# Performance work log

Measured on AMD Instinct MI355X. Metric: run time of the kernel, lower is better.

## Reference

```python
import jax, jax.numpy as jnp
import numpy as np

B, N, C = 8, 1024, 768
H, D = 12, 64  # num_heads, head_dim
SCALE = D ** -0.5


def setup_inputs() -> dict:
    key = jax.random.key(0)
    ks = jax.random.split(key, 6)
    x = jax.random.normal(ks[0], (B, N, C), dtype=jnp.float32)
    # per-head Linear weights stacked: [H, D, C] (torch Linear stores [out, in])
    Wq = jax.random.normal(ks[1], (H, D, C), dtype=jnp.float32) * 0.02
    Wk = jax.random.normal(ks[2], (H, D, C), dtype=jnp.float32) * 0.02
    Wv = jax.random.normal(ks[3], (H, D, C), dtype=jnp.float32) * 0.02
    Wp = jax.random.normal(ks[4], (C, C), dtype=jnp.float32) * 0.02
    bp = jnp.zeros((C,), dtype=jnp.float32)
    return {"x": x, "Wq": Wq, "Wk": Wk, "Wv": Wv, "Wp": Wp, "bp": bp}


def reference(x, Wq, Wk, Wv, Wp, bp):
    # Per-head projections (batched across heads): [B, H, N, D]
    q = jnp.einsum('bnc,hdc->bhnd', x, Wq) * SCALE
    k = jnp.einsum('bnc,hdc->bhnd', x, Wk)
    v = jnp.einsum('bnc,hdc->bhnd', x, Wv)
    # Scaled dot-product attention per head
    attn = jax.nn.softmax(jnp.einsum('bhnd,bhmd->bhnm', q, k), axis=-1)
    out = jnp.einsum('bhnm,bhmd->bhnd', attn, v)
    # Concat heads along last dim == transpose to [B, N, H, D] then reshape
    out = out.transpose(0, 2, 1, 3).reshape(x.shape[0], x.shape[1], -1)
    # Output projection
    return out @ Wp.T + bp
```

## Files before the change

kernel.cpp:

```cpp
#include <hip/hip_runtime.h>

typedef unsigned short u16;
typedef __attribute__((ext_vector_type(8))) __bf16 bf16x8;
typedef __attribute__((ext_vector_type(4))) float f32x4;

__device__ __forceinline__ u16 f2bf(float f) {
    union { float f; unsigned u; } v; v.f = f;
    unsigned u = v.u;
    u += 0x7FFFu + ((u >> 16) & 1u);
    return (u16)(u >> 16);
}

typedef const __attribute__((address_space(1))) void GV;
typedef __attribute__((address_space(3))) void LV;
__device__ __forceinline__ void gl2lds16(const void* g, void* l) {
    __builtin_amdgcn_global_load_lds((GV*)g, (LV*)l, 16, 0, 0);
}

__global__ __launch_bounds__(256) void cast_all(
    const float* __restrict__ x,  const float* __restrict__ Wq,
    const float* __restrict__ Wk, const float* __restrict__ Wv,
    const float* __restrict__ Wp,
    u16* __restrict__ xb, u16* __restrict__ wb, u16* __restrict__ wpb)
{
    int bid = blockIdx.x;
    const float4* s; ushort4* d; int idx;
    if (bid < 6144) {
        s = (const float4*)x; d = (ushort4*)xb; idx = bid * 256 + threadIdx.x;
    } else {
        int t = bid - 6144;
        int w = t / 576;
        idx = (t - w * 576) * 256 + threadIdx.x;
        s = (const float4*)(w == 0 ? Wq : w == 1 ? Wk : w == 2 ? Wv : Wp);
        d = (ushort4*)(w == 3 ? wpb : wb + w * 589824);
    }
    float4 f = s[idx];
    ushort4 o;
    o.x = f2bf(f.x); o.y = f2bf(f.y); o.z = f2bf(f.z); o.w = f2bf(f.w);
    d[idx] = o;
}

__device__ __forceinline__ void stage_tile64(const u16* src, int k0, u16* lds, int tid) {
    #pragma unroll
    for (int h = 0; h < 4; h++) {
        int i = h * 256 + tid;
        int row = i >> 3, p = i & 7;
        int l = p ^ (row & 7);
        gl2lds16(src + (size_t)row * 768 + k0 + l * 8, lds + i * 8);
    }
}
__device__ __forceinline__ const bf16x8* frag64(const u16* lds, int row, int kc) {
    return reinterpret_cast<const bf16x8*>(lds + row * 64 + ((kc ^ (row & 7)) * 8));
}

__global__ __launch_bounds__(256, 2) void gemm_qkv(
    const u16* __restrict__ A, const u16* __restrict__ Bm,
    u16* __restrict__ qo, u16* __restrict__ ko, u16* __restrict__ vto)
{
    __shared__ u16 As[8192];
    __shared__ u16 Bs[8192];
    const int tid = threadIdx.x;
    const int wave = tid >> 6, lane = tid & 63;
    const int quad = lane >> 4, l16 = lane & 15;
    const int wr = (wave >> 1) * 64, wc = (wave & 1) * 64;
    const int rowBase = blockIdx.y * 128;
    const int colBase = blockIdx.x * 128;

    f32x4 acc[4][4] = {};
    const u16* aSrc = A + (size_t)rowBase * 768;
    const u16* bSrc = Bm + (size_t)colBase * 768;

    for (int k0 = 0; k0 < 768; k0 += 64) {
        __syncthreads();
        stage_tile64(aSrc, k0, As, tid);
        stage_tile64(bSrc, k0, Bs, tid);
        __syncthreads();
        #pragma unroll
        for (int ks = 0; ks < 2; ks++) {
            bf16x8 a[4], b[4];
            #pragma unroll
            for (int mi = 0; mi < 4; mi++)
                a[mi] = *frag64(As, wr + mi * 16 + l16, ks * 4 + quad);
            #pragma unroll
            for (int ni = 0; ni < 4; ni++)
                b[ni] = *frag64(Bs, wc + ni * 16 + l16, ks * 4 + quad);
            #pragma unroll
            for (int mi = 0; mi < 4; mi++)
                #pragma unroll
                for (int ni = 0; ni < 4; ni++)
                    acc[mi][ni] = __builtin_amdgcn_mfma_f32_16x16x32_bf16(a[mi], b[ni], acc[mi][ni], 0, 0, 0);
        }
    }

    #pragma unroll
    for (int mi = 0; mi < 4; mi++) {
        #pragma unroll
        for (int ni = 0; ni < 4; ni++) {
            int gj = colBase + wc + ni * 16 + l16;
            int which = gj / 768;
            int r = gj - which * 768;
            int h = r >> 6, d = r & 63;
            int gi0 = rowBase + wr + mi * 16 + quad * 4;
            int b_ = gi0 >> 10;
            int n0 = gi0 & 1023;
            if (which == 2) {
                ushort4 pk;
                pk.x = f2bf(acc[mi][ni][0]);
                pk.y = f2bf(acc[mi][ni][1]);
                pk.z = f2bf(acc[mi][ni][2]);
                pk.w = f2bf(acc[mi][ni][3]);
                *reinterpret_cast<ushort4*>(vto + ((size_t)(b_ * 12 + h) * 64 + d) * 1024 + n0) = pk;
            } else {
                float s = (which == 0) ? 0.125f : 1.0f;
                u16* dst = (which == 0 ? qo : ko) + ((size_t)(b_ * 12 + h) * 1024 + n0) * 64 + d;
                #pragma unroll
                for (int rr = 0; rr < 4; rr++)
                    dst[(size_t)rr * 64] = f2bf(acc[mi][ni][rr] * s);
            }
        }
    }
}

__global__ __launch_bounds__(256, 3) void attn_fwd(
    const u16* __restrict__ q, const u16* __restrict__ k,
    const u16* __restrict__ vt, u16* __restrict__ ao)
{
    __shared__ u16 Ks[2][4096];
    __shared__ u16 Vs[2][4096];
    __shared__ u16 Ps[128][72];
    const int bh = blockIdx.x, qt = blockIdx.y;
    const int b = bh / 12, h = bh - b * 12;
    const int tid = threadIdx.x;
    const int wave = tid >> 6, lane = tid & 63;
    const int quad = lane >> 4, l16 = lane & 15;
    const int swz = l16 & 7;
    u16 (*PsW)[72] = &Ps[wave * 32];

    const u16* qb = q + (size_t)bh * 65536 + ((size_t)qt * 128 + wave * 32) * 64;
    const u16* kb = k + (size_t)bh * 65536;
    const u16* vb = vt + (size_t)bh * 65536;

    auto stage = [&](int buf, int j0) {
        #pragma unroll
        for (int r = 0; r < 2; r++) {
            int i = r * 256 + tid;
            int row = i >> 3, cp = i & 7;
            int cl = cp ^ (row & 7);
            gl2lds16((const char*)kb + (size_t)(j0 + row) * 128 + cl * 16,
                     (char*)&Ks[buf][0] + i * 16);
        }
        #pragma unroll
        for (int r = 0; r < 2; r++) {
            int i = r * 256 + tid;
            int row = i >> 3, cp = i & 7;
            int cl = cp ^ (row & 7);
            gl2lds16((const char*)vb + (size_t)row * 2048 + (size_t)j0 * 2 + cl * 16,
                     (char*)&Vs[buf][0] + i * 16);
        }
    };

    stage(0, 0);

    bf16x8 qf[2][2];
    #pragma unroll
    for (int ni = 0; ni < 2; ni++)
        #pragma unroll
        for (int ks = 0; ks < 2; ks++)
            qf[ni][ks] = *reinterpret_cast<const bf16x8*>(qb + (ni * 16 + l16) * 64 + ks * 32 + quad * 8);

    f32x4 o[2][4] = {};
    float lsum[2] = {0.f, 0.f};

    __syncthreads();

    int buf = 0;
    for (int j0 = 0; j0 < 1024; j0 += 64) {
        if (j0 + 64 < 1024) stage(buf ^ 1, j0 + 64);

        f32x4 s[4][2] = {};
        #pragma unroll
        for (int ks = 0; ks < 2; ks++) {
            bf16x8 kf[4];
            #pragma unroll
            for (int mi = 0; mi < 4; mi++) {
                int row = mi * 16 + l16;
                int ch = (ks * 4 + quad) ^ swz;
                kf[mi] = *reinterpret_cast<const bf16x8*>(&Ks[buf][row * 64 + ch * 8]);
            }
            #pragma unroll
            for (int mi = 0; mi < 4; mi++)
                #pragma unroll
                for (int ni = 0; ni < 2; ni++)
                    s[mi][ni] = __builtin_amdgcn_mfma_f32_16x16x32_bf16(kf[mi], qf[ni][ks], s[mi][ni], 0, 0, 0);
        }

        #pragma unroll
        for (int mi = 0; mi < 4; mi++) {
            #pragma unroll
            for (int ni = 0; ni < 2; ni++) {
                float p0 = __expf(s[mi][ni][0]);
                float p1 = __expf(s[mi][ni][1]);
                float p2 = __expf(s[mi][ni][2]);
                float p3 = __expf(s[mi][ni][3]);
                lsum[ni] += (p0 + p1) + (p2 + p3);
                ushort4 pk;
                pk.x = f2bf(p0); pk.y = f2bf(p1); pk.z = f2bf(p2); pk.w = f2bf(p3);
                *reinterpret_cast<ushort4*>(&PsW[ni * 16 + l16][mi * 16 + quad * 4]) = pk;
            }
        }

        #pragma unroll
        for (int ks = 0; ks < 2; ks++) {
            bf16x8 vf[4], pf[2];
            #pragma unroll
            for (int di = 0; di < 4; di++) {
                int row = di * 16 + l16;
                int ch = (ks * 4 + quad) ^ swz;
                vf[di] = *reinterpret_cast<const bf16x8*>(&Vs[buf][row * 64 + ch * 8]);
            }
            #pragma unroll
            for (int mi = 0; mi < 2; mi++)
                pf[mi] = *reinterpret_cast<const bf16x8*>(&PsW[mi * 16 + l16][ks * 32 + quad * 8]);
            #pragma unroll
            for (int mi = 0; mi < 2; mi++)
                #pragma unroll
                for (int di = 0; di < 4; di++)
                    o[mi][di] = __builtin_amdgcn_mfma_f32_16x16x32_bf16(pf[mi], vf[di], o[mi][di], 0, 0, 0);
        }

        __syncthreads();
        buf ^= 1;
    }

    #pragma unroll
    for (int ni = 0; ni < 2; ni++) {
        lsum[ni] += __shfl_xor(lsum[ni], 16, 64);
        lsum[ni] += __shfl_xor(lsum[ni], 32, 64);
    }

    #pragma unroll
    for (int mi = 0; mi < 2; mi++) {
        #pragma unroll
        for (int r = 0; r < 4; r++) {
            float lv = __shfl(lsum[mi], quad * 4 + r, 16);
            float inv = 1.0f / lv;
            int n = qt * 128 + wave * 32 + mi * 16 + quad * 4 + r;
            size_t base = (size_t)(b * 1024 + n) * 768 + h * 64;
            #pragma unroll
            for (int di = 0; di < 4; di++)
                ao[base + di * 16 + l16] = f2bf(o[mi][di][r] * inv);
        }
    }
}

__global__ __launch_bounds__(256, 2) void gemm_proj(
    const u16* __restrict__ A, const u16* __restrict__ Bm,
    const float* __restrict__ bias, float* __restrict__ out)
{
    __shared__ u16 As[8192];
    __shared__ u16 Bs[8192];
    const int tid = threadIdx.x;
    const int wave = tid >> 6, lane = tid & 63;
    const int quad = lane >> 4, l16 = lane & 15;
    const int wr = (wave >> 1) * 64, wc = (wave & 1) * 64;
    const int rowBase = blockIdx.y * 128;
    const int colBase = blockIdx.x * 128;

    f32x4 acc[4][4] = {};
    const u16* aSrc = A + (size_t)rowBase * 768;
    const u16* bSrc = Bm + (size_t)colBase * 768;

    for (int k0 = 0; k0 < 768; k0 += 64) {
        __syncthreads();
        stage_tile64(aSrc, k0, As, tid);
        stage_tile64(bSrc, k0, Bs, tid);
        __syncthreads();
        #pragma unroll
        for (int ks = 0; ks < 2; ks++) {
            bf16x8 a[4], b[4];
            #pragma unroll
            for (int mi = 0; mi < 4; mi++)
                a[mi] = *frag64(As, wr + mi * 16 + l16, ks * 4 + quad);
            #pragma unroll
            for (int ni = 0; ni < 4; ni++)
                b[ni] = *frag64(Bs, wc + ni * 16 + l16, ks * 4 + quad);
            #pragma unroll
            for (int mi = 0; mi < 4; mi++)
                #pragma unroll
                for (int ni = 0; ni < 4; ni++)
                    acc[mi][ni] = __builtin_amdgcn_mfma_f32_16x16x32_bf16(a[mi], b[ni], acc[mi][ni], 0, 0, 0);
        }
    }

    #pragma unroll
    for (int mi = 0; mi < 4; mi++) {
        #pragma unroll
        for (int ni = 0; ni < 4; ni++) {
            int gj = colBase + wc + ni * 16 + l16;
            float bv = bias[gj];
            int gi0 = rowBase + wr + mi * 16 + quad * 4;
            #pragma unroll
            for (int rr2 = 0; rr2 < 4; rr2++)
                out[(size_t)(gi0 + rr2) * 768 + gj] = acc[mi][ni][rr2] + bv;
        }
    }
}

extern "C" void kernel_launch(void* const* d_in, const int* in_sizes, int n_in,
                              void* d_out, int out_size, void* d_ws, size_t ws_size,
                              hipStream_t stream) {
    const float* x  = (const float*)d_in[0];
    const float* Wq = (const float*)d_in[1];
    const float* Wk = (const float*)d_in[2];
    const float* Wv = (const float*)d_in[3];
    const float* Wp = (const float*)d_in[4];
    const float* bp = (const float*)d_in[5];
    float* out = (float*)d_out;

    u16* xb  = (u16*)d_ws;
    u16* wb  = xb  + 6291456;
    u16* wpb = wb  + 1769472;
    u16* qo  = wpb + 589824;
    u16* ko  = qo  + 6291456;
    u16* vto = ko  + 6291456;
    u16* ao  = vto + 6291456;

    cast_all<<<8448, 256, 0, stream>>>(x, Wq, Wk, Wv, Wp, xb, wb, wpb);
    gemm_qkv<<<dim3(18, 64), 256, 0, stream>>>(xb, wb, qo, ko, vto);
    attn_fwd<<<dim3(96, 8), 256, 0, stream>>>(qo, ko, vto, ao);
    gemm_proj<<<dim3(6, 64), 256, 0, stream>>>(ao, wpb, bp, out);
}
```

Measured before the change: 186.8 us.

## Triple-buffer GEMM K-loop with async LDS loads and single barrier

Replaces the synchronous 64-wide K staging in both QKV and projection GEMMs with a three-stage ring of 32-wide K tiles loaded via global_load_lds. Prefetch runs two tiles ahead, gated by vmcnt waits and one barrier per step. This is meant to hide global load latency behind MFMA work. The smaller per-stage LDS footprint also allows raising the launch bound to 3 blocks per CU. Correctness depends on the hand-written vmcnt counts and on a single barrier being enough to protect buffer reuse.

```diff
diff --git a/kernel.cpp b/kernel.cpp
--- a/kernel.cpp
+++ b/kernel.cpp
@@ -40,25 +40,62 @@
     d[idx] = o;
 }
 
-__device__ __forceinline__ void stage_tile64(const u16* src, int k0, u16* lds, int tid) {
-    #pragma unroll
-    for (int h = 0; h < 4; h++) {
+__device__ __forceinline__ void stage32(const u16* src, int k0, u16* lds, int tid) {
+    #pragma unroll
+    for (int h = 0; h < 2; h++) {
         int i = h * 256 + tid;
-        int row = i >> 3, p = i & 7;
-        int l = p ^ (row & 7);
-        gl2lds16(src + (size_t)row * 768 + k0 + l * 8, lds + i * 8);
-    }
-}
-__device__ __forceinline__ const bf16x8* frag64(const u16* lds, int row, int kc) {
-    return reinterpret_cast<const bf16x8*>(lds + row * 64 + ((kc ^ (row & 7)) * 8));
-}
-
-__global__ __launch_bounds__(256, 2) void gemm_qkv(
+        int line = i >> 3, pos = i & 7;
+        int p = pos ^ (line & 7);
+        int r = line * 2 + (p >> 2), c = p & 3;
+        gl2lds16(src + (size_t)r * 768 + k0 + c * 8, lds + i * 8);
+    }
+}
+__device__ __forceinline__ const bf16x8* frag32(const u16* lds, int row, int c) {
+    int line = row >> 1;
+    int pos = (((row & 1) << 2) | c) ^ (line & 7);
+    return reinterpret_cast<const bf16x8*>(lds + line * 64 + pos * 8);
+}
+
+__device__ __forceinline__ void gemm_kloop(
+    const u16* __restrict__ aSrc, const u16* __restrict__ bSrc,
+    u16 (&As)[3][4096], u16 (&Bs)[3][4096], f32x4 (&acc)[4][4],
+    int tid, int wr, int wc, int quad, int l16)
+{
+    stage32(aSrc, 0,  As[0], tid); stage32(bSrc, 0,  Bs[0], tid);
+    stage32(aSrc, 32, As[1], tid); stage32(bSrc, 32, Bs[1], tid);
+    int buf = 0;
+    for (int t = 0; t < 24; t++) {
+        if (t == 23) asm volatile("s_waitcnt vmcnt(0)" ::: "memory");
+        else         asm volatile("s_waitcnt vmcnt(4)" ::: "memory");
+        __builtin_amdgcn_s_barrier();
+        asm volatile("" ::: "memory");
+        bf16x8 a[4], b[4];
+        #pragma unroll
+        for (int mi = 0; mi < 4; mi++)
+            a[mi] = *frag32(As[buf], wr + mi * 16 + l16, quad);
+        #pragma unroll
+        for (int ni = 0; ni < 4; ni++)
+            b[ni] = *frag32(Bs[buf], wc + ni * 16 + l16, quad);
+        #pragma unroll
+        for (int mi = 0; mi < 4; mi++)
+            #pragma unroll
+            for (int ni = 0; ni < 4; ni++)
+                acc[mi][ni] = __builtin_amdgcn_mfma_f32_16x16x32_bf16(a[mi], b[ni], acc[mi][ni], 0, 0, 0);
+        if (t + 2 < 24) {
+            int sb = buf + 2; if (sb >= 3) sb -= 3;
+            stage32(aSrc, (t + 2) * 32, As[sb], tid);
+            stage32(bSrc, (t + 2) * 32, Bs[sb], tid);
+        }
+        buf = (buf == 2) ? 0 : buf + 1;
+    }
+}
+
+__global__ __launch_bounds__(256, 3) void gemm_qkv(
     const u16* __restrict__ A, const u16* __restrict__ Bm,
     u16* __restrict__ qo, u16* __restrict__ ko, u16* __restrict__ vto)
 {
-    __shared__ u16 As[8192];
-    __shared__ u16 Bs[8192];
+    __shared__ u16 As[3][4096];
+    __shared__ u16 Bs[3][4096];
     const int tid = threadIdx.x;
     const int wave = tid >> 6, lane = tid & 63;
     const int quad = lane >> 4, l16 = lane & 15;
@@ -67,30 +104,8 @@
     const int colBase = blockIdx.x * 128;
 
     f32x4 acc[4][4] = {};
-    const u16* aSrc = A + (size_t)rowBase * 768;
-    const u16* bSrc = Bm + (size_t)colBase * 768;
-
-    for (int k0 = 0; k0 < 768; k0 += 64) {
-        __syncthreads();
-        stage_tile64(aSrc, k0, As, tid);
-        stage_tile64(bSrc, k0, Bs, tid);
-        __syncthreads();
-        #pragma unroll
-        for (int ks = 0; ks < 2; ks++) {
-            bf16x8 a[4], b[4];
-            #pragma unroll
-            for (int mi = 0; mi < 4; mi++)
-                a[mi] = *frag64(As, wr + mi * 16 + l16, ks * 4 + quad);
-            #pragma unroll
-            for (int ni = 0; ni < 4; ni++)
-                b[ni] = *frag64(Bs, wc + ni * 16 + l16, ks * 4 + quad);
-            #pragma unroll
-            for (int mi = 0; mi < 4; mi++)
-                #pragma unroll
-                for (int ni = 0; ni < 4; ni++)
-                    acc[mi][ni] = __builtin_amdgcn_mfma_f32_16x16x32_bf16(a[mi], b[ni], acc[mi][ni], 0, 0, 0);
-        }
-    }
+    gemm_kloop(A + (size_t)rowBase * 768, Bm + (size_t)colBase * 768,
+               As, Bs, acc, tid, wr, wc, quad, l16);
 
     #pragma unroll
     for (int mi = 0; mi < 4; mi++) {
@@ -253,12 +268,12 @@
     }
 }
 
-__global__ __launch_bounds__(256, 2) void gemm_proj(
+__global__ __launch_bounds__(256, 3) void gemm_proj(
     const u16* __restrict__ A, const u16* __restrict__ Bm,
     const float* __restrict__ bias, float* __restrict__ out)
 {
-    __shared__ u16 As[8192];
-    __shared__ u16 Bs[8192];
+    __shared__ u16 As[3][4096];
+    __shared__ u16 Bs[3][4096];
     const int tid = threadIdx.x;
     const int wave = tid >> 6, lane = tid & 63;
     const int quad = lane >> 4, l16 = lane & 15;
@@ -267,30 +282,8 @@
     const int colBase = blockIdx.x * 128;
 
     f32x4 acc[4][4] = {};
-    const u16* aSrc = A + (size_t)rowBase * 768;
-    const u16* bSrc = Bm + (size_t)colBase * 768;
-
-    for (int k0 = 0; k0 < 768; k0 += 64) {
-        __syncthreads();
-        stage_tile64(aSrc, k0, As, tid);
-        stage_tile64(bSrc, k0, Bs, tid);
-        __syncthreads();
-        #pragma unroll
-        for (int ks = 0; ks < 2; ks++) {
-            bf16x8 a[4], b[4];
-            #pragma unroll
-            for (int mi = 0; mi < 4; mi++)
-                a[mi] = *frag64(As, wr + mi * 16 + l16, ks * 4 + quad);
-            #pragma unroll
-            for (int ni = 0; ni < 4; ni++)
-                b[ni] = *frag64(Bs, wc + ni * 16 + l16, ks * 4 + quad);
-            #pragma unroll
-            for (int mi = 0; mi < 4; mi++)
-                #pragma unroll
-                for (int ni = 0; ni < 4; ni++)
-                    acc[mi][ni] = __builtin_amdgcn_mfma_f32_16x16x32_bf16(a[mi], b[ni], acc[mi][ni], 0, 0, 0);
-        }
-    }
+    gemm_kloop(A + (size_t)rowBase * 768, Bm + (size_t)colBase * 768,
+               As, Bs, acc, tid, wr, wc, quad, l16);
 
     #pragma unroll
     for (int mi = 0; mi < 4; mi++) {
```

Result: no change. 190.5 us (+2.0%).

## Use 256x128 tiles with triple-buffered async LDS pipeline in both GEMMs

Applied to the files above, without the earlier changes.

Both projection GEMMs move from 128x128 tiles with 256 threads and a synchronous load/compute loop to 256x128 tiles with 512 threads and a three-stage LDS ring buffer. Global-to-LDS loads for tile t+2 are issued in the middle of the MFMA work on tile t, with explicit vmcnt waits and raw barriers in place of __syncthreads. MFMA sections are wrapped in s_setprio to favour the compute waves. This is meant to hide memory latency and halve the number of blocks. The cost is 144KB of LDS per block, which limits occupancy, and hand-tuned waitcnt counts that must exactly match the number of outstanding loads.

```diff
diff --git a/kernel.cpp b/kernel.cpp
--- a/kernel.cpp
+++ b/kernel.cpp
@@ -40,67 +40,113 @@
     d[idx] = o;
 }
 
-__device__ __forceinline__ void stage_tile64(const u16* src, int k0, u16* lds, int tid) {
-    #pragma unroll
-    for (int h = 0; h < 4; h++) {
-        int i = h * 256 + tid;
-        int row = i >> 3, p = i & 7;
-        int l = p ^ (row & 7);
-        gl2lds16(src + (size_t)row * 768 + k0 + l * 8, lds + i * 8);
-    }
+__device__ __forceinline__ void stage_g(const u16* src, int k0, u16* lds, int g, int tid) {
+    int i = g * 512 + tid;
+    int row = i >> 3, p = i & 7;
+    int l = p ^ (row & 7);
+    gl2lds16(src + (size_t)row * 768 + k0 + l * 8, lds + i * 8);
 }
 __device__ __forceinline__ const bf16x8* frag64(const u16* lds, int row, int kc) {
     return reinterpret_cast<const bf16x8*>(lds + row * 64 + ((kc ^ (row & 7)) * 8));
 }
 
-__global__ __launch_bounds__(256, 2) void gemm_qkv(
+__device__ __forceinline__ void kloop256(
+    const u16* __restrict__ aSrc, const u16* __restrict__ bSrc,
+    u16* As, u16* Bs, f32x4 (&acc)[4][4],
+    int tid, int wm, int wn, int quad, int l16)
+{
+    #pragma unroll
+    for (int tt = 0; tt < 2; tt++) {
+        #pragma unroll
+        for (int g = 0; g < 4; g++) stage_g(aSrc, tt * 64, As + tt * 16384, g, tid);
+        #pragma unroll
+        for (int g = 0; g < 2; g++) stage_g(bSrc, tt * 64, Bs + tt * 8192, g, tid);
+    }
+    asm volatile("s_waitcnt vmcnt(6)" ::: "memory");
+    __builtin_amdgcn_s_barrier();
+    asm volatile("" ::: "memory");
+
+    int buf = 0;
+    for (int t = 0; t < 12; t++) {
+        const u16* Ab = As + buf * 16384;
+        const u16* Bb = Bs + buf * 8192;
+        int sb = buf + 2; if (sb >= 3) sb -= 3;
+        u16* Asb = As + sb * 16384;
+        u16* Bsb = Bs + sb * 8192;
+        const bool pf = (t + 2 < 12);
+        const int k2 = (t + 2) * 64;
+
+        bf16x8 a[4], b[4];
+        #pragma unroll
+        for (int mi = 0; mi < 4; mi++) a[mi] = *frag64(Ab, wm * 64 + mi * 16 + l16, quad);
+        #pragma unroll
+        for (int ni = 0; ni < 4; ni++) b[ni] = *frag64(Bb, wn * 64 + ni * 16 + l16, quad);
+        if (pf) {
+            stage_g(aSrc, k2, Asb, 0, tid);
+            stage_g(aSrc, k2, Asb, 1, tid);
+            stage_g(aSrc, k2, Asb, 2, tid);
+        }
+        __builtin_amdgcn_s_barrier();
+        asm volatile("" ::: "memory");
+        __builtin_amdgcn_s_setprio(1);
+        #pragma unroll
+        for (int mi = 0; mi < 4; mi++)
+            #pragma unroll
+            for (int ni = 0; ni < 4; ni++)
+                acc[mi][ni] = __builtin_amdgcn_mfma_f32_16x16x32_bf16(a[mi], b[ni], acc[mi][ni], 0, 0, 0);
+        __builtin_amdgcn_s_setprio(0);
+
+        #pragma unroll
+        for (int mi = 0; mi < 4; mi++) a[mi] = *frag64(Ab, wm * 64 + mi * 16 + l16, 4 + quad);
+        #pragma unroll
+        for (int ni = 0; ni < 4; ni++) b[ni] = *frag64(Bb, wn * 64 + ni * 16 + l16, 4 + quad);
+        if (pf) {
+            stage_g(aSrc, k2, Asb, 3, tid);
+            stage_g(bSrc, k2, Bsb, 0, tid);
+            stage_g(bSrc, k2, Bsb, 1, tid);
+        }
+        if (t <= 9)       asm volatile("s_waitcnt vmcnt(6)" ::: "memory");
+        else if (t == 10) asm volatile("s_waitcnt vmcnt(0)" ::: "memory");
+        __builtin_amdgcn_s_barrier();
+        asm volatile("" ::: "memory");
+        __builtin_amdgcn_s_setprio(1);
+        #pragma unroll
+        for (int mi = 0; mi < 4; mi++)
+            #pragma unroll
+            for (int ni = 0; ni < 4; ni++)
+                acc[mi][ni] = __builtin_amdgcn_mfma_f32_16x16x32_bf16(a[mi], b[ni], acc[mi][ni], 0, 0, 0);
+        __builtin_amdgcn_s_setprio(0);
+
+        buf++; if (buf == 3) buf = 0;
+    }
+}
+
+__global__ __launch_bounds__(512, 2) void gemm_qkv(
     const u16* __restrict__ A, const u16* __restrict__ Bm,
     u16* __restrict__ qo, u16* __restrict__ ko, u16* __restrict__ vto)
 {
-    __shared__ u16 As[8192];
-    __shared__ u16 Bs[8192];
+    __shared__ u16 As[3][16384];
+    __shared__ u16 Bs[3][8192];
     const int tid = threadIdx.x;
     const int wave = tid >> 6, lane = tid & 63;
     const int quad = lane >> 4, l16 = lane & 15;
-    const int wr = (wave >> 1) * 64, wc = (wave & 1) * 64;
-    const int rowBase = blockIdx.y * 128;
+    const int wm = wave >> 1, wn = wave & 1;
+    const int rowBase = blockIdx.y * 256;
     const int colBase = blockIdx.x * 128;
 
     f32x4 acc[4][4] = {};
-    const u16* aSrc = A + (size_t)rowBase * 768;
-    const u16* bSrc = Bm + (size_t)colBase * 768;
-
-    for (int k0 = 0; k0 < 768; k0 += 64) {
-        __syncthreads();
-        stage_tile64(aSrc, k0, As, tid);
-        stage_tile64(bSrc, k0, Bs, tid);
-        __syncthreads();
-        #pragma unroll
-        for (int ks = 0; ks < 2; ks++) {
-            bf16x8 a[4], b[4];
-            #pragma unroll
-            for (int mi = 0; mi < 4; mi++)
-                a[mi] = *frag64(As, wr + mi * 16 + l16, ks * 4 + quad);
-            #pragma unroll
-            for (int ni = 0; ni < 4; ni++)
-                b[ni] = *frag64(Bs, wc + ni * 16 + l16, ks * 4 + quad);
-            #pragma unroll
-            for (int mi = 0; mi < 4; mi++)
-                #pragma unroll
-                for (int ni = 0; ni < 4; ni++)
-                    acc[mi][ni] = __builtin_amdgcn_mfma_f32_16x16x32_bf16(a[mi], b[ni], acc[mi][ni], 0, 0, 0);
-        }
-    }
+    kloop256(A + (size_t)rowBase * 768, Bm + (size_t)colBase * 768,
+             &As[0][0], &Bs[0][0], acc, tid, wm, wn, quad, l16);
 
     #pragma unroll
     for (int mi = 0; mi < 4; mi++) {
         #pragma unroll
         for (int ni = 0; ni < 4; ni++) {
-            int gj = colBase + wc + ni * 16 + l16;
+            int gj = colBase + wn * 64 + ni * 16 + l16;
             int which = gj / 768;
             int r = gj - which * 768;
             int h = r >> 6, d = r & 63;
-            int gi0 = rowBase + wr + mi * 16 + quad * 4;
+            int gi0 = rowBase + wm * 64 + mi * 16 + quad * 4;
             int b_ = gi0 >> 10;
             int n0 = gi0 & 1023;
             if (which == 2) {
@@ -253,52 +299,30 @@
     }
 }
 
-__global__ __launch_bounds__(256, 2) void gemm_proj(
+__global__ __launch_bounds__(512, 2) void gemm_proj(
     const u16* __restrict__ A, const u16* __restrict__ Bm,
     const float* __restrict__ bias, float* __restrict__ out)
 {
-    __shared__ u16 As[8192];
-    __shared__ u16 Bs[8192];
+    __shared__ u16 As[3][16384];
+    __shared__ u16 Bs[3][8192];
     const int tid = threadIdx.x;
     const int wave = tid >> 6, lane = tid & 63;
     const int quad = lane >> 4, l16 = lane & 15;
-    const int wr = (wave >> 1) * 64, wc = (wave & 1) * 64;
-    const int rowBase = blockIdx.y * 128;
+    const int wm = wave >> 1, wn = wave & 1;
+    const int rowBase = blockIdx.y * 256;
     const int colBase = blockIdx.x * 128;
 
     f32x4 acc[4][4] = {};
-    const u16* aSrc = A + (size_t)rowBase * 768;
-    const u16* bSrc = Bm + (size_t)colBase * 768;
-
-    for (int k0 = 0; k0 < 768; k0 += 64) {
-        __syncthreads();
-        stage_tile64(aSrc, k0, As, tid);
-        stage_tile64(bSrc, k0, Bs, tid);
-        __syncthreads();
-        #pragma unroll
-        for (int ks = 0; ks < 2; ks++) {
-            bf16x8 a[4], b[4];
-            #pragma unroll
-            for (int mi = 0; mi < 4; mi++)
-                a[mi] = *frag64(As, wr + mi * 16 + l16, ks * 4 + quad);
-            #pragma unroll
-            for (int ni = 0; ni < 4; ni++)
-                b[ni] = *frag64(Bs, wc + ni * 16 + l16, ks * 4 + quad);
-            #pragma unroll
-            for (int mi = 0; mi < 4; mi++)
-                #pragma unroll
-                for (int ni = 0; ni < 4; ni++)
-                    acc[mi][ni] = __builtin_amdgcn_mfma_f32_16x16x32_bf16(a[mi], b[ni], acc[mi][ni], 0, 0, 0);
-        }
-    }
+    kloop256(A + (size_t)rowBase * 768, Bm + (size_t)colBase * 768,
+             &As[0][0], &Bs[0][0], acc, tid, wm, wn, quad, l16);
 
     #pragma unroll
     for (int mi = 0; mi < 4; mi++) {
         #pragma unroll
         for (int ni = 0; ni < 4; ni++) {
-            int gj = colBase + wc + ni * 16 + l16;
+            int gj = colBase + wn * 64 + ni * 16 + l16;
             float bv = bias[gj];
-            int gi0 = rowBase + wr + mi * 16 + quad * 4;
+            int gi0 = rowBase + wm * 64 + mi * 16 + quad * 4;
             #pragma unroll
             for (int rr2 = 0; rr2 < 4; rr2++)
                 out[(size_t)(gi0 + rr2) * 768 + gj] = acc[mi][ni][rr2] + bv;
@@ -326,7 +350,7 @@
     u16* ao  = vto + 6291456;
 
     cast_all<<<8448, 256, 0, stream>>>(x, Wq, Wk, Wv, Wp, xb, wb, wpb);
-    gemm_qkv<<<dim3(18, 64), 256, 0, stream>>>(xb, wb, qo, ko, vto);
+    gemm_qkv<<<dim3(18, 32), 512, 0, stream>>>(xb, wb, qo, ko, vto);
     attn_fwd<<<dim3(96, 8), 256, 0, stream>>>(qo, ko, vto, ao);
-    gemm_proj<<<dim3(6, 64), 256, 0, stream>>>(ao, wpb, bp, out);
-}
+    gemm_proj<<<dim3(6, 32), 512, 0, stream>>>(ao, wpb, bp, out);
+}
```

New measurement: 190.3 us. Within noise of the previous version (+1.9%).
